# Optimization experiments

Measured on AMD Instinct MI355X. Metric: run time of the kernel, lower is better.

## Reference

```python
import jax, jax.numpy as jnp
import numpy as np

N_IMG = 8
IMG_H = IMG_W = 1024
STRIDES = (4, 8, 16, 32, 64)
FEAT = tuple(IMG_H // s for s in STRIDES)
RATIOS = (0.5, 1.0, 2.0)
A = len(RATIOS)
PRE_NMS = 1000
POST_NMS = 1000
NMS_THRESH = 0.7
SCORE_THRESH = 0.0
MIN_SIZE = 1e-3
BBOX_CLIP = float(np.log(1000.0 / 16.0))  # torchvision bbox_xform_clip
NPL = tuple(f * f * A for f in FEAT)      # anchors per level


def _make_anchors():
    levels = []
    for stride, f in zip(STRIDES, FEAT):
        size = stride * 8.0
        base = []
        for r in RATIOS:
            w = size * np.sqrt(1.0 / r)
            h = size * np.sqrt(r)
            base.append([-w / 2, -h / 2, w / 2, h / 2])
        base = np.asarray(base, np.float32)              # [A,4]
        coords = np.arange(f, dtype=np.float32) * stride
        sy, sx = np.meshgrid(coords, coords, indexing="ij")
        shifts = np.stack([sx, sy, sx, sy], -1).reshape(-1, 1, 4)  # y-major, matches [H,W,A] flatten
        levels.append((shifts + base[None]).reshape(-1, 4))
    return np.concatenate(levels, 0).astype(np.float32)


def setup_inputs() -> dict:
    key = jax.random.key(0)
    ks = jax.random.split(key, 10)
    inp = {}
    for i, f in enumerate(FEAT):
        inp[f"obj_l{i}"] = jax.random.normal(ks[i], (N_IMG, A, f, f), jnp.float32)
        inp[f"delta_l{i}"] = jax.random.normal(ks[5 + i], (N_IMG, A * 4, f, f), jnp.float32) * 0.2
    inp["anchors"] = jnp.asarray(_make_anchors())
    return inp


def _flatten_level(obj, delta):
    # permute_and_flatten: [N,A,H,W] -> [N,H*W*A] ; [N,A*4,H,W] -> [N,H*W*A,4]
    n, a, h, w = obj.shape
    o = jnp.transpose(obj, (0, 2, 3, 1)).reshape(n, -1)
    d = jnp.transpose(delta.reshape(n, a, 4, h, w), (0, 3, 4, 1, 2)).reshape(n, -1, 4)
    return o, d


def _decode(deltas, anchors):
    # BoxCoder(weights=(1,1,1,1)).decode
    w = anchors[:, 2] - anchors[:, 0]
    h = anchors[:, 3] - anchors[:, 1]
    cx = anchors[:, 0] + 0.5 * w
    cy = anchors[:, 1] + 0.5 * h
    dx, dy = deltas[..., 0], deltas[..., 1]
    dw = jnp.minimum(deltas[..., 2], BBOX_CLIP)
    dh = jnp.minimum(deltas[..., 3], BBOX_CLIP)
    pcx = dx * w + cx
    pcy = dy * h + cy
    pw = jnp.exp(dw) * w
    ph = jnp.exp(dh) * h
    return jnp.stack([pcx - 0.5 * pw, pcy - 0.5 * ph, pcx + 0.5 * pw, pcy + 0.5 * ph], -1)


def _nms_image(boxes, scores, lvl):
    # clip_boxes_to_image
    x1 = jnp.clip(boxes[:, 0], 0.0, IMG_W)
    y1 = jnp.clip(boxes[:, 1], 0.0, IMG_H)
    x2 = jnp.clip(boxes[:, 2], 0.0, IMG_W)
    y2 = jnp.clip(boxes[:, 3], 0.0, IMG_H)
    boxes = jnp.stack([x1, y1, x2, y2], -1)
    # remove_small_boxes + score_thresh, as a mask (fixed shapes)
    valid = (x2 - x1 >= MIN_SIZE) & (y2 - y1 >= MIN_SIZE) & (scores >= SCORE_THRESH)
    s = jnp.where(valid, scores, -1.0)
    order = jnp.argsort(-s)
    boxes, s, valid, lvl = boxes[order], s[order], valid[order], lvl[order]
    # batched_nms: offset boxes per level so cross-level IoU is 0
    ob = boxes + (lvl.astype(boxes.dtype) * (max(IMG_H, IMG_W) + 1.0))[:, None]
    ob = jax.lax.stop_gradient(ob)  # keep decisions are non-differentiable
    area = (ob[:, 2] - ob[:, 0]) * (ob[:, 3] - ob[:, 1])
    lt = jnp.maximum(ob[:, None, :2], ob[None, :, :2])
    rb = jnp.minimum(ob[:, None, 2:], ob[None, :, 2:])
    wh = jnp.maximum(rb - lt, 0.0)
    inter = wh[..., 0] * wh[..., 1]
    iou = inter / (area[:, None] + area[None, :] - inter + 1e-9)  # [K,K]
    k = boxes.shape[0]
    jidx = jnp.arange(k)

    def body(i, keep):
        sup = keep[i] & (iou[i] > NMS_THRESH) & (jidx > i)
        return keep & ~sup

    keep = jax.lax.fori_loop(0, k, body, valid)
    # compact kept boxes (score-sorted) into fixed [POST_NMS] output, zero-padded
    rank = jnp.cumsum(keep) - 1
    tgt = jnp.where(keep & (rank < POST_NMS), rank, POST_NMS)
    out_b = jnp.zeros((POST_NMS + 1, 4), boxes.dtype).at[tgt].set(boxes)[:POST_NMS]
    out_s = jnp.zeros((POST_NMS + 1,), s.dtype).at[tgt].set(jnp.where(keep, s, 0.0))[:POST_NMS]
    return out_b, out_s


def _forward(objs, deltas, anchors):
    flat = [_flatten_level(o, d) for o, d in zip(objs, deltas)]
    obj = jnp.concatenate([f[0] for f in flat], 1)       # [N, K_total]
    dl = jnp.concatenate([f[1] for f in flat], 1)        # [N, K_total, 4]
    proposals = _decode(dl, anchors)                     # [N, K_total, 4]
    lvl_full = jnp.concatenate([jnp.full((n,), i, jnp.int32) for i, n in enumerate(NPL)])
    # per-level top-k on objectness logits
    idxs, off = [], 0
    for n in NPL:
        kk = min(PRE_NMS, n)
        _, ti = jax.lax.top_k(obj[:, off:off + n], kk)
        idxs.append(ti + off)
        off += n
    top_idx = jnp.concatenate(idxs, 1)                   # [N, K_sel]
    scores = jax.nn.sigmoid(jnp.take_along_axis(obj, top_idx, 1))
    prop = jnp.take_along_axis(proposals, top_idx[..., None], 1)
    lvl = lvl_full[top_idx]
    boxes_out, _ = jax.lax.map(lambda t: _nms_image(*t), (prop, scores, lvl))
    return boxes_out                                     # [N, POST_NMS, 4]


def reference(obj_l0, obj_l1, obj_l2, obj_l3, obj_l4, delta_l0, delta_l1, delta_l2, delta_l3, delta_l4, anchors):
    return _forward([obj_l0, obj_l1, obj_l2, obj_l3, obj_l4],
                    [delta_l0, delta_l1, delta_l2, delta_l3, delta_l4], anchors)
```

## Files before the change

### kernel.cpp

```cpp
#include <hip/hip_runtime.h>
#include <cstdint>

#define K_SEL 4768
#define NBIN 4096
#define BUFCAP 512
#define SLICE 512
#define TPAD 9216

struct P5 { const float* p[5]; };

__device__ __forceinline__ unsigned fsortkey(float f) {
  unsigned b = __float_as_uint(f);
  return (b & 0x80000000u) ? ~b : (b | 0x80000000u);
}

__global__ __launch_bounds__(256) void k_hist(P5 obj, unsigned* phist) {
  int p = blockIdx.y; int img = p / 5, lvl = p % 5;
  int f = 256 >> lvl; int n = 3 * f * f;
  __shared__ unsigned lh[NBIN];
  for (int b = threadIdx.x; b < NBIN; b += 256) lh[b] = 0;
  __syncthreads();
  const float4* src4 = (const float4*)(obj.p[lvl] + (size_t)img * n);
  int n4 = n >> 2;
  int chunk = (n4 + gridDim.x - 1) / gridDim.x;
  int e0 = blockIdx.x * chunk, e1 = min(n4, e0 + chunk);
  for (int e = e0 + threadIdx.x; e < e1; e += 256) {
    float4 v = src4[e];
    atomicAdd(&lh[fsortkey(v.x) >> 20], 1u);
    atomicAdd(&lh[fsortkey(v.y) >> 20], 1u);
    atomicAdd(&lh[fsortkey(v.z) >> 20], 1u);
    atomicAdd(&lh[fsortkey(v.w) >> 20], 1u);
  }
  __syncthreads();
  unsigned* dst = phist + ((size_t)(p * 8 + blockIdx.x)) * NBIN;
  for (int b = threadIdx.x; b < NBIN; b += 256) dst[b] = lh[b];
}

__global__ __launch_bounds__(256) void k_thresh(const unsigned* phist, int* Bthr) {
  int p = blockIdx.x; int lvl = p % 5;
  unsigned kk = (lvl == 4) ? 768u : 1000u;
  __shared__ unsigned hsum[NBIN];
  __shared__ unsigned csum[256];
  int c = threadIdx.x;
  unsigned tot[16];
#pragma unroll
  for (int k = 0; k < 16; ++k) tot[k] = 0;
  for (int g = 0; g < 8; ++g) {
    const unsigned* hp = phist + ((size_t)(p * 8 + g)) * NBIN + c * 16;
#pragma unroll
    for (int k = 0; k < 16; ++k) tot[k] += hp[k];
  }
  unsigned s = 0;
#pragma unroll
  for (int k = 0; k < 16; ++k) { hsum[c * 16 + k] = tot[k]; s += tot[k]; }
  csum[c] = s;
  __syncthreads();
  if (c == 0) {
    unsigned acc = 0; int B = 0;
    for (int cc = 255; cc >= 0; --cc) {
      if (acc + csum[cc] >= kk) {
        for (int b = 15; b >= 0; --b) {
          acc += hsum[cc * 16 + b];
          if (acc >= kk) { B = cc * 16 + b; break; }
        }
        break;
      }
      acc += csum[cc];
    }
    Bthr[p] = B;
  }
}

__global__ __launch_bounds__(256) void k_gather(P5 obj, const int* Bthr,
                                                unsigned* cntB, unsigned long long* ck) {
  int p = blockIdx.y; int img = p / 5, lvl = p % 5;
  int f = 256 >> lvl; int hw = f * f; int n = 3 * hw;
  int B = Bthr[p];
  int tid = threadIdx.x;
  int lane = tid & 63, wv = tid >> 6;
  int shift = 2 * (8 - lvl);
  const float4* src4 = (const float4*)(obj.p[lvl] + (size_t)img * n);
  int n4 = n >> 2;
  int chunk = (n4 + 31) >> 5;
  int e0 = blockIdx.x * chunk, e1 = min(n4, e0 + chunk);
  __shared__ unsigned long long buf[4][BUFCAP];
  __shared__ unsigned wTot[4];
  unsigned wc = 0;
  for (int e = e0 + tid; e < e1; e += 256) {
    float4 v = src4[e];
    float vv[4] = {v.x, v.y, v.z, v.w};
#pragma unroll
    for (int j = 0; j < 4; ++j) {
      unsigned sv = fsortkey(vv[j]);
      bool pass = (int)(sv >> 20) >= B;
      unsigned long long m = __ballot(pass);
      if (m) {
        if (pass) {
          unsigned pos = wc + (unsigned)__popcll(m & ((1ULL << lane) - 1ULL));
          int ee = e * 4 + j;
          int a = ee >> shift;
          int r = ee & (hw - 1);
          unsigned kidx = (unsigned)(r * 3 + a);
          unsigned long long key = ((unsigned long long)sv << 32) | (0xFFFFFFFFu - kidx);
          if (pos < BUFCAP) buf[wv][pos] = key;
        }
        wc += (unsigned)__popcll(m);
      }
    }
  }
  if (lane == 0) wTot[wv] = min(wc, (unsigned)BUFCAP);
  __syncthreads();
  unsigned myOff = 0;
  for (int x = 0; x < wv; ++x) myOff += wTot[x];
  unsigned tot4 = wTot[0] + wTot[1] + wTot[2] + wTot[3];
  unsigned long long* dst = ck + ((size_t)p * 32 + blockIdx.x) * SLICE;
  for (unsigned j = lane; j < wTot[wv]; j += 64) {
    unsigned gp = myOff + j;
    if (gp < SLICE) dst[gp] = buf[wv][j];
  }
  if (tid == 0) cntB[p * 32 + blockIdx.x] = min(tot4, (unsigned)SLICE);
}

__global__ __launch_bounds__(256) void k_seldec(P5 del, const float* anchors,
                                                const unsigned* cntB,
                                                const unsigned long long* ck,
                                                float* boxP, unsigned long long* keyP) {
  int p = blockIdx.y; int img = p / 5, lvl = p % 5;
  int kk = (lvl == 4) ? 768 : 1000;
  int soff = lvl * 1000;
  int tid = threadIdx.x;
  __shared__ unsigned long long sk[4096];
  __shared__ unsigned offs[33];
  if (tid < 32) {
    unsigned v = cntB[p * 32 + tid];
#pragma unroll
    for (int d = 1; d < 32; d <<= 1) {
      unsigned o = __shfl(v, tid - d);
      if (tid >= d) v += o;
    }
    offs[tid + 1] = v;
    if (tid == 0) offs[0] = 0;
  }
  __syncthreads();
  int Cc = min((int)offs[32], 4096);
  if (blockIdx.x * 256 >= Cc) return;
  for (int x = tid; x < Cc; x += 256) {
    int lo = 0;
#pragma unroll
    for (int d = 16; d; d >>= 1)
      if (offs[lo + d] <= (unsigned)x) lo += d;
    sk[x] = ck[((size_t)p * 32 + lo) * SLICE + (x - offs[lo])];
  }
  __syncthreads();
  int c = blockIdx.x * 256 + tid;
  if (c >= Cc) return;
  unsigned long long kc = sk[c];
  unsigned k = 0xFFFFFFFFu - (unsigned)kc;
  unsigned sv = (unsigned)(kc >> 32);
  int f = 256 >> lvl, hw = f * f;
  const int aoffA[5] = {0, 196608, 245760, 258048, 261120};
  int a = (int)(k % 3u); int r = (int)(k / 3u);
  int y = r >> (8 - lvl); int x = r & (f - 1);
  const float* dp = del.p[lvl] + (size_t)(img * 12 + a * 4) * hw + (size_t)y * f + x;
  float d0 = dp[0], d1 = dp[hw], d2 = dp[2 * hw], d3 = dp[3 * hw];
  const float* ar = anchors + (size_t)(aoffA[lvl] + (int)k) * 4;
  float a0 = ar[0], a1 = ar[1], a2 = ar[2], a3 = ar[3];
  int rank = 0;
#pragma unroll 8
  for (int j = 0; j < Cc; ++j) rank += (sk[j] > kc) ? 1 : 0;
  if (rank >= kk) return;
  int i = soff + rank;
  int slot = img * K_SEL + i;
  float w = __fsub_rn(a2, a0), h = __fsub_rn(a3, a1);
  float cx = __fadd_rn(a0, __fmul_rn(0.5f, w));
  float cy = __fadd_rn(a1, __fmul_rn(0.5f, h));
  const float CLIP = 4.135166556742356f;
  float dw = fminf(d2, CLIP), dh = fminf(d3, CLIP);
  float pcx = __fadd_rn(__fmul_rn(d0, w), cx);
  float pcy = __fadd_rn(__fmul_rn(d1, h), cy);
  float pw = __fmul_rn(expf(dw), w);
  float ph = __fmul_rn(expf(dh), h);
  float x1 = __fsub_rn(pcx, __fmul_rn(0.5f, pw));
  float y1 = __fsub_rn(pcy, __fmul_rn(0.5f, ph));
  float x2 = __fadd_rn(pcx, __fmul_rn(0.5f, pw));
  float y2 = __fadd_rn(pcy, __fmul_rn(0.5f, ph));
  float x1c = fminf(fmaxf(x1, 0.0f), 1024.0f);
  float y1c = fminf(fmaxf(y1, 0.0f), 1024.0f);
  float x2c = fminf(fmaxf(x2, 0.0f), 1024.0f);
  float y2c = fminf(fmaxf(y2, 0.0f), 1024.0f);
  bool valid = (__fsub_rn(x2c, x1c) >= 1e-3f) && (__fsub_rn(y2c, y1c) >= 1e-3f);
  float* bp = boxP + (size_t)slot * 4;
  bp[0] = x1c; bp[1] = y1c; bp[2] = x2c; bp[3] = y2c;
  unsigned low = 0xFFFFFFFFu - (unsigned)i;
  keyP[slot] = valid ? (((unsigned long long)sv << 32) | low) : (unsigned long long)low;
}

__device__ __forceinline__ bool iou_gt(float rx1, float ry1, float rx2, float ry2, float rar,
                                       float cx1, float cy1, float cx2, float cy2, float car) {
  float ltx = fmaxf(rx1, cx1), lty = fmaxf(ry1, cy1);
  float rbx = fminf(rx2, cx2), rby = fminf(ry2, cy2);
  float wx = fmaxf(__fsub_rn(rbx, ltx), 0.0f);
  float wy = fmaxf(__fsub_rn(rby, lty), 0.0f);
  float inter = __fmul_rn(wx, wy);
  float denom = __fadd_rn(__fsub_rn(__fadd_rn(rar, car), inter), 1e-9f);
  return __fdiv_rn(inter, denom) > 0.7f;
}

__global__ __launch_bounds__(64) void k_lvlmask(const float* boxP, unsigned long long* T) {
  int img = blockIdx.y;
  int q = blockIdx.x;
  int lvl, q2;
  if (q < 544) { lvl = q / 136; q2 = q - lvl * 136; }
  else         { lvl = 4;       q2 = q - 544; }
  int kk = (lvl == 4) ? 768 : 1000;
  int nch = (kk + 63) >> 6;
  int rb = 0;
  while (q2 >= nch - rb) { q2 -= nch - rb; ++rb; }
  int cb = rb + q2;
  int t = threadIdx.x;
  float off = __fmul_rn((float)lvl, 1025.0f);
  const float4* b4 = (const float4*)boxP + (size_t)img * K_SEL + lvl * 1000;
  __shared__ float rx1s[64], ry1s[64], rx2s[64], ry2s[64], rars[64];
  int j = rb * 64 + t;
  if (j < kk) {
    float4 bb = b4[j];
    float ox1 = __fadd_rn(bb.x, off), oy1 = __fadd_rn(bb.y, off);
    float ox2 = __fadd_rn(bb.z, off), oy2 = __fadd_rn(bb.w, off);
    rx1s[t] = ox1; ry1s[t] = oy1; rx2s[t] = ox2; ry2s[t] = oy2;
    rars[t] = __fmul_rn(__fsub_rn(ox2, ox1), __fsub_rn(oy2, oy1));
  }
  __syncthreads();
  int i = cb * 64 + t;
  if (i >= kk) return;
  float4 bb = b4[i];
  float cx1 = __fadd_rn(bb.x, off), cy1 = __fadd_rn(bb.y, off);
  float cx2 = __fadd_rn(bb.z, off), cy2 = __fadd_rn(bb.w, off);
  float car = __fmul_rn(__fsub_rn(cx2, cx1), __fsub_rn(cy2, cy1));
  int jmaxR = min(64, kk - rb * 64);
  int jend = (rb == cb) ? min(t, jmaxR) : jmaxR;
  unsigned long long bits = 0;
  for (int jj = 0; jj < jend; ++jj) {
    if (iou_gt(rx1s[jj], ry1s[jj], rx2s[jj], ry2s[jj], rars[jj], cx1, cy1, cx2, cy2, car))
      bits |= (1ULL << jj);
  }
  const int Pt[16] = {0, 1, 4, 7, 12, 17, 24, 31, 40, 49, 60, 71, 84, 97, 112, 127};
  int sc = (cb + 1) | 1;
  T[(size_t)(img * 5 + lvl) * TPAD + 64 * Pt[cb] + t * sc + rb] = bits;
}

__global__ __launch_bounds__(256) void k_lvlnms(const unsigned long long* keyP,
                                                const unsigned long long* Tg_,
                                                unsigned long long* keepw) {
  int p = blockIdx.x; int img = p / 5, lvl = p % 5;
  int kk = (lvl == 4) ? 768 : 1000;
  int tw = (lvl == 4) ? 5376 : TPAD;
  int tid = threadIdx.x;
  __shared__ __align__(16) unsigned long long Ts[TPAD];
  const unsigned long long* Tg = Tg_ + (size_t)p * TPAD;
  const unsigned long long* kp = keyP + (size_t)img * K_SEL + lvl * 1000;
  unsigned vmask = 0;
  if (tid < 64) {
#pragma unroll
    for (int c = 0; c < 16; ++c) {
      int i = c * 64 + tid;
      bool v = (i < kk) && ((kp[min(i, kk - 1)] >> 32) != 0ULL);
      vmask |= v ? (1u << c) : 0u;
    }
  }
  {
    const ulonglong2* Tg2 = (const ulonglong2*)Tg;
    ulonglong2* Ts2 = (ulonglong2*)Ts;
    int nv = tw >> 1;
    for (int x = tid; x < nv; x += 1024) {
      int x1i = x + 256, x2i = x + 512, x3i = x + 768;
      ulonglong2 a0 = Tg2[x], a1 = {}, a2 = {}, a3 = {};
      if (x1i < nv) a1 = Tg2[x1i];
      if (x2i < nv) a2 = Tg2[x2i];
      if (x3i < nv) a3 = Tg2[x3i];
      Ts2[x] = a0;
      if (x1i < nv) Ts2[x1i] = a1;
      if (x2i < nv) Ts2[x2i] = a2;
      if (x3i < nv) Ts2[x3i] = a3;
    }
  }
  __syncthreads();
  if (tid >= 64) return;
  int t = tid;
  const int Pt[16] = {0, 1, 4, 7, 12, 17, 24, 31, 40, 49, 60, 71, 84, 97, 112, 127};
  unsigned long long kw[16];
#pragma unroll
  for (int w = 0; w < 16; ++w) kw[w] = 0ULL;
#pragma unroll
  for (int c = 0; c < 16; ++c) {
    if (c * 64 < kk) {
      int base = 64 * Pt[c] + t * ((c + 1) | 1);
      unsigned long long tv[16];
#pragma unroll
      for (int w = 0; w < 16; ++w) tv[w] = Ts[base + w];
      unsigned long long a = 0;
#pragma unroll
      for (int w = 0; w < 16; ++w) a |= tv[w] & kw[w];
      unsigned long long colT = tv[c];
      bool alive = ((vmask >> c) & 1u) && (a == 0ULL);
      unsigned long long keepm = 0ULL;
      unsigned long long actm = __ballot(alive);
      while (actm) {
        bool cank = alive && ((colT & actm) == 0ULL);
        unsigned long long newk = __ballot(cank);
        keepm |= newk;
        alive = alive && !cank && ((colT & newk) == 0ULL);
        actm = __ballot(alive);
      }
      kw[c] = keepm;
    }
  }
  if (t == 0) {
#pragma unroll
    for (int c = 0; c < 16; ++c) keepw[(size_t)p * 16 + c] = kw[c];
  }
}

__global__ __launch_bounds__(256) void k_merge(const unsigned long long* keyP, const float* boxP,
                                               const unsigned long long* keepw, float* out) {
  int p = blockIdx.x; int img = p / 5, lvl = p % 5;
  int tid = threadIdx.x;
  __shared__ unsigned long long lkey[5000];
  __shared__ int lpos[5000];
  __shared__ int wp[5][17];
  __shared__ unsigned long long kwS[80];
  for (int x = tid; x < 80; x += 256) {
    kwS[x] = keepw[(size_t)img * 80 + x];
  }
  __syncthreads();
  if (tid < 5) {
    int acc = 0;
    for (int w = 0; w < 16; ++w) { wp[tid][w] = acc; acc += (int)__popcll(kwS[tid * 16 + w]); }
    wp[tid][16] = acc;
  }
  __syncthreads();
  const unsigned long long* kp = keyP + (size_t)img * K_SEL;
  for (int i = tid; i < K_SEL; i += 256) {
    int l = (i < 4000) ? i / 1000 : 4;
    int li = i - l * 1000;
    unsigned long long wmask = kwS[l * 16 + (li >> 6)];
    if ((wmask >> (li & 63)) & 1ULL) {
      int j = wp[l][li >> 6] + (int)__popcll(wmask & ((1ULL << (li & 63)) - 1ULL));
      lkey[l * 1000 + j] = kp[i];
      lpos[l * 1000 + j] = i;
    }
  }
  __syncthreads();
  const float4* b4 = (const float4*)boxP + (size_t)img * K_SEL;
  float4* out4 = (float4*)out + (size_t)img * 1000;
  int kn = wp[lvl][16];
  for (int j = tid; j < kn; j += 256) {
    unsigned long long key = lkey[lvl * 1000 + j];
    int grank = j;
#pragma unroll
    for (int l2 = 0; l2 < 5; ++l2) {
      if (l2 == lvl) continue;
      int lo = 0, hi = wp[l2][16];
      const unsigned long long* a = &lkey[l2 * 1000];
      while (lo < hi) { int mid = (lo + hi) >> 1; if (a[mid] > key) lo = mid + 1; else hi = mid; }
      grank += lo;
    }
    if (grank < 1000) out4[grank] = b4[lpos[lvl * 1000 + j]];
  }
  if (lvl == 0) {
    int KT = wp[0][16] + wp[1][16] + wp[2][16] + wp[3][16] + wp[4][16];
    for (int s = min(KT, 1000) + tid; s < 1000; s += 256)
      out4[s] = make_float4(0.f, 0.f, 0.f, 0.f);
  }
}

extern "C" void kernel_launch(void* const* d_in, const int* in_sizes, int n_in,
                              void* d_out, int out_size, void* d_ws, size_t ws_size,
                              hipStream_t stream) {
  (void)in_sizes; (void)n_in;
  P5 obj, del;
  for (int i = 0; i < 5; ++i) {
    obj.p[i] = (const float*)d_in[2 * i];
    del.p[i] = (const float*)d_in[2 * i + 1];
  }
  const float* anchors = (const float*)d_in[10];
  float* out = (float*)d_out;
  char* ws = (char*)d_ws;

  unsigned* cntB              = (unsigned*)(ws + 0);
  int* Bthr                   = (int*)(ws + 5120);
  unsigned long long* candK   = (unsigned long long*)(ws + 8192);
  float* boxP                 = (float*)(ws + 5548544);
  unsigned long long* keyP    = (unsigned long long*)(ws + 6158848);
  unsigned long long* keepw   = (unsigned long long*)(ws + 6464000);
  unsigned long long* T       = (unsigned long long*)(ws + 6469120);
  unsigned* phist             = (unsigned*)(ws + 6469120);
  const size_t NEED = 11712000ULL;
  if (ws_size < NEED) { hipMemsetAsync(d_out, 0, (size_t)out_size * 4, stream); return; }

  k_hist    <<<dim3(8, 40), 256, 0, stream>>>(obj, phist);
  k_thresh  <<<40, 256, 0, stream>>>(phist, Bthr);
  k_gather  <<<dim3(32, 40), 256, 0, stream>>>(obj, Bthr, cntB, candK);
  k_seldec  <<<dim3(16, 40), 256, 0, stream>>>(del, anchors, cntB, candK, boxP, keyP);
  k_lvlmask <<<dim3(622, 8), 64, 0, stream>>>(boxP, T);
  k_lvlnms  <<<40, 256, 0, stream>>>(keyP, T, keepw);
  k_merge   <<<40, 256, 0, stream>>>(keyP, boxP, keepw, out);
}
```

Baseline: 203.8 us.

## Replace O(C^2) rank counting with histogram-bucketed counting sort in seldec

The selection kernel used to rank each candidate by comparing it against all other candidates, an O(C^2) scan repeated across 16 blocks per image-level. It now exports cumulative coarse-histogram counts from the threshold kernel and builds a finer sub-histogram for the boundary bin inside seldec. Candidates are scattered into buckets so each one only compares against its own bucket. The launch drops to one block per image-level with 18 candidates per thread held in registers, which lowers parallelism and raises register and LDS pressure.

```diff
diff --git a/kernel.cpp b/kernel.cpp
--- a/kernel.cpp
+++ b/kernel.cpp
@@ -5,6 +5,8 @@
 #define NBIN 4096
 #define BUFCAP 512
 #define SLICE 512
+#define CAP 4608
+#define CPT 18
 #define TPAD 9216
 
 struct P5 { const float* p[5]; };
@@ -36,11 +38,13 @@
   for (int b = threadIdx.x; b < NBIN; b += 256) dst[b] = lh[b];
 }
 
-__global__ __launch_bounds__(256) void k_thresh(const unsigned* phist, int* Bthr) {
+__global__ __launch_bounds__(256) void k_thresh(const unsigned* phist, int* Bthr,
+                                                unsigned* cumA) {
   int p = blockIdx.x; int lvl = p % 5;
   unsigned kk = (lvl == 4) ? 768u : 1000u;
   __shared__ unsigned hsum[NBIN];
   __shared__ unsigned csum[256];
+  __shared__ unsigned sAb[256];
   int c = threadIdx.x;
   unsigned tot[16];
 #pragma unroll
@@ -68,6 +72,16 @@
       acc += csum[cc];
     }
     Bthr[p] = B;
+    unsigned a2 = 0;
+    for (int cc = 255; cc >= 0; --cc) { sAb[cc] = a2; a2 += csum[cc]; }
+  }
+  __syncthreads();
+  unsigned run = sAb[c];
+  unsigned* cg = cumA + (size_t)p * NBIN;
+  for (int k = 15; k >= 0; --k) {
+    int bin = c * 16 + k;
+    cg[bin] = run;
+    run += hsum[bin];
   }
 }
 
@@ -122,15 +136,21 @@
 }
 
 __global__ __launch_bounds__(256) void k_seldec(P5 del, const float* anchors,
+                                                const int* Bthr, const unsigned* cumA,
                                                 const unsigned* cntB,
                                                 const unsigned long long* ck,
                                                 float* boxP, unsigned long long* keyP) {
-  int p = blockIdx.y; int img = p / 5, lvl = p % 5;
+  int p = blockIdx.x; int img = p / 5, lvl = p % 5;
   int kk = (lvl == 4) ? 768 : 1000;
   int soff = lvl * 1000;
   int tid = threadIdx.x;
-  __shared__ unsigned long long sk[4096];
+  __shared__ unsigned long long skS[CAP];
+  __shared__ unsigned cur1[NBIN];
+  __shared__ unsigned h2[NBIN];
+  __shared__ unsigned part[256];
   __shared__ unsigned offs[33];
+  const unsigned* cA = cumA + (size_t)p * NBIN;
+  for (int x = tid; x < NBIN; x += 256) { cur1[x] = cA[x]; h2[x] = 0u; }
   if (tid < 32) {
     unsigned v = cntB[p * 32 + tid];
 #pragma unroll
@@ -142,57 +162,121 @@
     if (tid == 0) offs[0] = 0;
   }
   __syncthreads();
-  int Cc = min((int)offs[32], 4096);
-  if (blockIdx.x * 256 >= Cc) return;
-  for (int x = tid; x < Cc; x += 256) {
-    int lo = 0;
-#pragma unroll
-    for (int d = 16; d; d >>= 1)
-      if (offs[lo + d] <= (unsigned)x) lo += d;
-    sk[x] = ck[((size_t)p * 32 + lo) * SLICE + (x - offs[lo])];
-  }
-  __syncthreads();
-  int c = blockIdx.x * 256 + tid;
-  if (c >= Cc) return;
-  unsigned long long kc = sk[c];
-  unsigned k = 0xFFFFFFFFu - (unsigned)kc;
-  unsigned sv = (unsigned)(kc >> 32);
-  int f = 256 >> lvl, hw = f * f;
-  const int aoffA[5] = {0, 196608, 245760, 258048, 261120};
-  int a = (int)(k % 3u); int r = (int)(k / 3u);
-  int y = r >> (8 - lvl); int x = r & (f - 1);
-  const float* dp = del.p[lvl] + (size_t)(img * 12 + a * 4) * hw + (size_t)y * f + x;
-  float d0 = dp[0], d1 = dp[hw], d2 = dp[2 * hw], d3 = dp[3 * hw];
-  const float* ar = anchors + (size_t)(aoffA[lvl] + (int)k) * 4;
-  float a0 = ar[0], a1 = ar[1], a2 = ar[2], a3 = ar[3];
-  int rank = 0;
-#pragma unroll 8
-  for (int j = 0; j < Cc; ++j) rank += (sk[j] > kc) ? 1 : 0;
-  if (rank >= kk) return;
-  int i = soff + rank;
-  int slot = img * K_SEL + i;
-  float w = __fsub_rn(a2, a0), h = __fsub_rn(a3, a1);
-  float cx = __fadd_rn(a0, __fmul_rn(0.5f, w));
-  float cy = __fadd_rn(a1, __fmul_rn(0.5f, h));
-  const float CLIP = 4.135166556742356f;
-  float dw = fminf(d2, CLIP), dh = fminf(d3, CLIP);
-  float pcx = __fadd_rn(__fmul_rn(d0, w), cx);
-  float pcy = __fadd_rn(__fmul_rn(d1, h), cy);
-  float pw = __fmul_rn(expf(dw), w);
-  float ph = __fmul_rn(expf(dh), h);
-  float x1 = __fsub_rn(pcx, __fmul_rn(0.5f, pw));
-  float y1 = __fsub_rn(pcy, __fmul_rn(0.5f, ph));
-  float x2 = __fadd_rn(pcx, __fmul_rn(0.5f, pw));
-  float y2 = __fadd_rn(pcy, __fmul_rn(0.5f, ph));
-  float x1c = fminf(fmaxf(x1, 0.0f), 1024.0f);
-  float y1c = fminf(fmaxf(y1, 0.0f), 1024.0f);
-  float x2c = fminf(fmaxf(x2, 0.0f), 1024.0f);
-  float y2c = fminf(fmaxf(y2, 0.0f), 1024.0f);
-  bool valid = (__fsub_rn(x2c, x1c) >= 1e-3f) && (__fsub_rn(y2c, y1c) >= 1e-3f);
-  float* bp = boxP + (size_t)slot * 4;
-  bp[0] = x1c; bp[1] = y1c; bp[2] = x2c; bp[3] = y2c;
-  unsigned low = 0xFFFFFFFFu - (unsigned)i;
-  keyP[slot] = valid ? (((unsigned long long)sv << 32) | low) : (unsigned long long)low;
+  int B = Bthr[p];
+  unsigned H = cA[B];
+  int Cc = min((int)offs[32], CAP);
+  unsigned long long key_[CPT];
+#pragma unroll
+  for (int k = 0; k < CPT; ++k) {
+    int x = tid + k * 256;
+    key_[k] = 0ULL;
+    if (x < Cc) {
+      int lo = 0;
+#pragma unroll
+      for (int d = 16; d; d >>= 1)
+        if (offs[lo + d] <= (unsigned)x) lo += d;
+      key_[k] = ck[((size_t)p * 32 + lo) * SLICE + (x - offs[lo])];
+    }
+  }
+#pragma unroll
+  for (int k = 0; k < CPT; ++k) {
+    int x = tid + k * 256;
+    if (x < Cc) {
+      unsigned sv = (unsigned)(key_[k] >> 32);
+      if ((int)(sv >> 20) == B) atomicAdd(&h2[(sv >> 8) & 0xFFFu], 1u);
+    }
+  }
+  __syncthreads();
+  {
+    unsigned s = 0;
+    for (int k2 = 0; k2 < 16; ++k2) s += h2[tid * 16 + k2];
+    part[tid] = s;
+    __syncthreads();
+    if (tid == 0) {
+      unsigned acc = 0;
+      for (int c = 255; c >= 0; --c) { unsigned t = part[c]; part[c] = acc; acc += t; }
+    }
+    __syncthreads();
+    unsigned run = part[tid];
+    for (int k2 = 15; k2 >= 0; --k2) {
+      unsigned hv = h2[tid * 16 + k2];
+      h2[tid * 16 + k2] = run;
+      run += hv;
+    }
+  }
+  __syncthreads();
+  int st_[CPT];
+#pragma unroll
+  for (int k = 0; k < CPT; ++k) {
+    int x = tid + k * 256;
+    st_[k] = 0;
+    if (x < Cc) {
+      unsigned sv = (unsigned)(key_[k] >> 32);
+      int b = (int)(sv >> 20);
+      st_[k] = (b == B) ? (int)(H + h2[(sv >> 8) & 0xFFFu]) : (int)cur1[b];
+    }
+  }
+  __syncthreads();
+  int pos_[CPT];
+#pragma unroll
+  for (int k = 0; k < CPT; ++k) {
+    int x = tid + k * 256;
+    pos_[k] = -1;
+    if (x < Cc) {
+      unsigned sv = (unsigned)(key_[k] >> 32);
+      int b = (int)(sv >> 20);
+      unsigned pos = (b == B) ? H + atomicAdd(&h2[(sv >> 8) & 0xFFFu], 1u)
+                              : atomicAdd(&cur1[b], 1u);
+      if (pos < (unsigned)CAP) { skS[pos] = key_[k]; pos_[k] = (int)pos; }
+    }
+  }
+  __syncthreads();
+#pragma unroll
+  for (int k = 0; k < CPT; ++k) {
+    if (pos_[k] < 0) continue;
+    unsigned long long kc = key_[k];
+    unsigned sv = (unsigned)(kc >> 32);
+    int b = (int)(sv >> 20);
+    int en = (b == B) ? (int)(H + h2[(sv >> 8) & 0xFFFu]) : (int)cur1[b];
+    if (en > CAP) en = CAP;
+    int st = st_[k];
+    int rank = st;
+    for (int j = st; j < en; ++j) rank += (skS[j] > kc) ? 1 : 0;
+    if (rank >= kk) continue;
+    unsigned kx = 0xFFFFFFFFu - (unsigned)kc;
+    int i = soff + rank;
+    int slot = img * K_SEL + i;
+    int f = 256 >> lvl, hw = f * f;
+    const int aoffA[5] = {0, 196608, 245760, 258048, 261120};
+    int a = (int)(kx % 3u); int r = (int)(kx / 3u);
+    int y = r >> (8 - lvl); int xi = r & (f - 1);
+    const float* dp = del.p[lvl] + (size_t)(img * 12 + a * 4) * hw + (size_t)y * f + xi;
+    float d0 = dp[0], d1 = dp[hw], d2 = dp[2 * hw], d3 = dp[3 * hw];
+    const float* ar = anchors + (size_t)(aoffA[lvl] + (int)kx) * 4;
+    float a0 = ar[0], a1 = ar[1], a2 = ar[2], a3 = ar[3];
+    float w = __fsub_rn(a2, a0), h = __fsub_rn(a3, a1);
+    float cx = __fadd_rn(a0, __fmul_rn(0.5f, w));
+    float cy = __fadd_rn(a1, __fmul_rn(0.5f, h));
+    const float CLIP = 4.135166556742356f;
+    float dw = fminf(d2, CLIP), dh = fminf(d3, CLIP);
+    float pcx = __fadd_rn(__fmul_rn(d0, w), cx);
+    float pcy = __fadd_rn(__fmul_rn(d1, h), cy);
+    float pw = __fmul_rn(expf(dw), w);
+    float ph = __fmul_rn(expf(dh), h);
+    float x1 = __fsub_rn(pcx, __fmul_rn(0.5f, pw));
+    float y1 = __fsub_rn(pcy, __fmul_rn(0.5f, ph));
+    float x2 = __fadd_rn(pcx, __fmul_rn(0.5f, pw));
+    float y2 = __fadd_rn(pcy, __fmul_rn(0.5f, ph));
+    float x1c = fminf(fmaxf(x1, 0.0f), 1024.0f);
+    float y1c = fminf(fmaxf(y1, 0.0f), 1024.0f);
+    float x2c = fminf(fmaxf(x2, 0.0f), 1024.0f);
+    float y2c = fminf(fmaxf(y2, 0.0f), 1024.0f);
+    bool valid = (__fsub_rn(x2c, x1c) >= 1e-3f) && (__fsub_rn(y2c, y1c) >= 1e-3f);
+    float* bp = boxP + (size_t)slot * 4;
+    bp[0] = x1c; bp[1] = y1c; bp[2] = x2c; bp[3] = y2c;
+    unsigned low = 0xFFFFFFFFu - (unsigned)i;
+    keyP[slot] = valid ? (((unsigned long long)sv << 32) | low) : (unsigned long long)low;
+  }
 }
 
 __device__ __forceinline__ bool iou_gt(float rx1, float ry1, float rx2, float ry2, float rar,
@@ -388,19 +472,20 @@
 
   unsigned* cntB              = (unsigned*)(ws + 0);
   int* Bthr                   = (int*)(ws + 5120);
-  unsigned long long* candK   = (unsigned long long*)(ws + 8192);
-  float* boxP                 = (float*)(ws + 5548544);
-  unsigned long long* keyP    = (unsigned long long*)(ws + 6158848);
-  unsigned long long* keepw   = (unsigned long long*)(ws + 6464000);
-  unsigned long long* T       = (unsigned long long*)(ws + 6469120);
-  unsigned* phist             = (unsigned*)(ws + 6469120);
-  const size_t NEED = 11712000ULL;
+  unsigned* cumA              = (unsigned*)(ws + 5376);
+  unsigned long long* candK   = (unsigned long long*)(ws + 663552);
+  float* boxP                 = (float*)(ws + 5906432);
+  unsigned long long* keyP    = (unsigned long long*)(ws + 6516736);
+  unsigned long long* keepw   = (unsigned long long*)(ws + 6821888);
+  unsigned long long* T       = (unsigned long long*)(ws + 6827008);
+  unsigned* phist             = (unsigned*)(ws + 6827008);
+  const size_t NEED = 12069888ULL;
   if (ws_size < NEED) { hipMemsetAsync(d_out, 0, (size_t)out_size * 4, stream); return; }
 
   k_hist    <<<dim3(8, 40), 256, 0, stream>>>(obj, phist);
-  k_thresh  <<<40, 256, 0, stream>>>(phist, Bthr);
+  k_thresh  <<<40, 256, 0, stream>>>(phist, Bthr, cumA);
   k_gather  <<<dim3(32, 40), 256, 0, stream>>>(obj, Bthr, cntB, candK);
-  k_seldec  <<<dim3(16, 40), 256, 0, stream>>>(del, anchors, cntB, candK, boxP, keyP);
+  k_seldec  <<<40, 256, 0, stream>>>(del, anchors, Bthr, cumA, cntB, candK, boxP, keyP);
   k_lvlmask <<<dim3(622, 8), 64, 0, stream>>>(boxP, T);
   k_lvlnms  <<<40, 256, 0, stream>>>(keyP, T, keepw);
   k_merge   <<<40, 256, 0, stream>>>(keyP, boxP, keepw, out);
```

Result: slower. 273.5 us (+34.2%).

## Add second-level radix histogram to shrink candidate set before rank selection

Applied to the files above, without the earlier changes.

Adds a k_thresh2 kernel that builds a finer 12-bit histogram over candidates falling in the boundary coarse bin, which gives a tighter threshold. k_seldec then compacts only the surviving candidates into shared memory before running the O(C^2) rank loop, and launches half as many blocks. The goal is to cut the quadratic rank-counting work and shared-memory footprint. The cost is an extra kernel launch and an extra pass reading the candidate keys.

```diff
diff --git a/kernel.cpp b/kernel.cpp
--- a/kernel.cpp
+++ b/kernel.cpp
@@ -5,6 +5,9 @@
 #define NBIN 4096
 #define BUFCAP 512
 #define SLICE 512
+#define CAPR 4608
+#define CPT 18
+#define CAP2 2048
 #define TPAD 9216
 
 struct P5 { const float* p[5]; };
@@ -36,7 +39,8 @@
   for (int b = threadIdx.x; b < NBIN; b += 256) dst[b] = lh[b];
 }
 
-__global__ __launch_bounds__(256) void k_thresh(const unsigned* phist, int* Bthr) {
+__global__ __launch_bounds__(256) void k_thresh(const unsigned* phist, int* Bthr,
+                                                unsigned* Hthr) {
   int p = blockIdx.x; int lvl = p % 5;
   unsigned kk = (lvl == 4) ? 768u : 1000u;
   __shared__ unsigned hsum[NBIN];
@@ -56,10 +60,11 @@
   csum[c] = s;
   __syncthreads();
   if (c == 0) {
-    unsigned acc = 0; int B = 0;
+    unsigned acc = 0, H = 0; int B = 0;
     for (int cc = 255; cc >= 0; --cc) {
       if (acc + csum[cc] >= kk) {
         for (int b = 15; b >= 0; --b) {
+          H = acc;
           acc += hsum[cc * 16 + b];
           if (acc >= kk) { B = cc * 16 + b; break; }
         }
@@ -68,6 +73,7 @@
       acc += csum[cc];
     }
     Bthr[p] = B;
+    Hthr[p] = H;
   }
 }
 
@@ -121,7 +127,66 @@
   if (tid == 0) cntB[p * 32 + blockIdx.x] = min(tot4, (unsigned)SLICE);
 }
 
+__global__ __launch_bounds__(256) void k_thresh2(const int* Bthr, const unsigned* Hthr,
+                                                 const unsigned* cntB,
+                                                 const unsigned long long* ck,
+                                                 int* B2thr, unsigned* Cc2g) {
+  int p = blockIdx.x; int lvl = p % 5;
+  unsigned kk = (lvl == 4) ? 768u : 1000u;
+  int B1 = Bthr[p];
+  unsigned H = Hthr[p];
+  unsigned kk2 = kk - H;
+  int tid = threadIdx.x;
+  __shared__ unsigned h2[NBIN];
+  __shared__ unsigned csum[256];
+  __shared__ unsigned offs[33];
+  for (int x = tid; x < NBIN; x += 256) h2[x] = 0;
+  if (tid < 32) {
+    unsigned v = cntB[p * 32 + tid];
+#pragma unroll
+    for (int d = 1; d < 32; d <<= 1) {
+      unsigned o = __shfl(v, tid - d);
+      if (tid >= d) v += o;
+    }
+    offs[tid + 1] = v;
+    if (tid == 0) offs[0] = 0;
+  }
+  __syncthreads();
+  int Cc = min((int)offs[32], CAPR);
+  for (int x = tid; x < Cc; x += 256) {
+    int lo = 0;
+#pragma unroll
+    for (int d = 16; d; d >>= 1)
+      if (offs[lo + d] <= (unsigned)x) lo += d;
+    unsigned long long key = ck[((size_t)p * 32 + lo) * SLICE + (x - offs[lo])];
+    unsigned sv = (unsigned)(key >> 32);
+    if ((int)(sv >> 20) == B1) atomicAdd(&h2[(sv >> 8) & 0xFFFu], 1u);
+  }
+  __syncthreads();
+  unsigned s = 0;
+  for (int k = 0; k < 16; ++k) s += h2[tid * 16 + k];
+  csum[tid] = s;
+  __syncthreads();
+  if (tid == 0) {
+    unsigned acc = 0; int B2 = 0;
+    for (int cc = 255; cc >= 0; --cc) {
+      if (acc + csum[cc] >= kk2) {
+        for (int b = 15; b >= 0; --b) {
+          acc += h2[cc * 16 + b];
+          if (acc >= kk2) { B2 = cc * 16 + b; break; }
+        }
+        break;
+      }
+      acc += csum[cc];
+    }
+    B2thr[p] = B2;
+    Cc2g[p] = H + acc;
+  }
+}
+
 __global__ __launch_bounds__(256) void k_seldec(P5 del, const float* anchors,
+                                                const int* Bthr, const int* B2thr,
+                                                const unsigned* Cc2g,
                                                 const unsigned* cntB,
                                                 const unsigned long long* ck,
                                                 float* boxP, unsigned long long* keyP) {
@@ -129,8 +194,12 @@
   int kk = (lvl == 4) ? 768 : 1000;
   int soff = lvl * 1000;
   int tid = threadIdx.x;
-  __shared__ unsigned long long sk[4096];
+  int lane = tid & 63, wv = tid >> 6;
+  unsigned Cc2 = min(Cc2g[p], (unsigned)CAP2);
+  if ((unsigned)(blockIdx.x * 256) >= Cc2) return;
+  __shared__ unsigned long long skc[CAP2];
   __shared__ unsigned offs[33];
+  __shared__ unsigned wsum[4];
   if (tid < 32) {
     unsigned v = cntB[p * 32 + tid];
 #pragma unroll
@@ -142,32 +211,61 @@
     if (tid == 0) offs[0] = 0;
   }
   __syncthreads();
-  int Cc = min((int)offs[32], 4096);
-  if (blockIdx.x * 256 >= Cc) return;
-  for (int x = tid; x < Cc; x += 256) {
-    int lo = 0;
-#pragma unroll
-    for (int d = 16; d; d >>= 1)
-      if (offs[lo + d] <= (unsigned)x) lo += d;
-    sk[x] = ck[((size_t)p * 32 + lo) * SLICE + (x - offs[lo])];
-  }
-  __syncthreads();
+  int B1 = Bthr[p], B2 = B2thr[p];
+  int Cc = min((int)offs[32], CAPR);
+  unsigned long long key_[CPT];
+  bool sur_[CPT];
+  unsigned myc = 0;
+#pragma unroll
+  for (int k = 0; k < CPT; ++k) {
+    int x = tid + k * 256;
+    key_[k] = 0ULL; sur_[k] = false;
+    if (x < Cc) {
+      int lo = 0;
+#pragma unroll
+      for (int d = 16; d; d >>= 1)
+        if (offs[lo + d] <= (unsigned)x) lo += d;
+      key_[k] = ck[((size_t)p * 32 + lo) * SLICE + (x - offs[lo])];
+      unsigned sv = (unsigned)(key_[k] >> 32);
+      int b = (int)(sv >> 20);
+      sur_[k] = (b > B1) || (b == B1 && (int)((sv >> 8) & 0xFFFu) >= B2);
+      myc += sur_[k] ? 1u : 0u;
+    }
+  }
+  unsigned v = myc;
+#pragma unroll
+  for (int d = 1; d < 64; d <<= 1) {
+    unsigned o = __shfl(v, lane - d);
+    if (lane >= d) v += o;
+  }
+  if (lane == 63) wsum[wv] = v;
+  __syncthreads();
+  unsigned base = 0;
+  for (int x = 0; x < wv; ++x) base += wsum[x];
+  unsigned pos = base + v - myc;
+  unsigned Ccc = wsum[0] + wsum[1] + wsum[2] + wsum[3];
+#pragma unroll
+  for (int k = 0; k < CPT; ++k) {
+    if (sur_[k]) { if (pos < (unsigned)CAP2) skc[pos] = key_[k]; ++pos; }
+  }
+  __syncthreads();
+  int Cs = min((int)Ccc, CAP2);
   int c = blockIdx.x * 256 + tid;
-  if (c >= Cc) return;
-  unsigned long long kc = sk[c];
-  unsigned k = 0xFFFFFFFFu - (unsigned)kc;
+  if (c >= Cs) return;
+  unsigned long long kc = skc[c];
+  unsigned kx = 0xFFFFFFFFu - (unsigned)kc;
   unsigned sv = (unsigned)(kc >> 32);
   int f = 256 >> lvl, hw = f * f;
   const int aoffA[5] = {0, 196608, 245760, 258048, 261120};
-  int a = (int)(k % 3u); int r = (int)(k / 3u);
-  int y = r >> (8 - lvl); int x = r & (f - 1);
-  const float* dp = del.p[lvl] + (size_t)(img * 12 + a * 4) * hw + (size_t)y * f + x;
+  int a = (int)(kx % 3u); int r = (int)(kx / 3u);
+  int y = r >> (8 - lvl); int xi = r & (f - 1);
+  const float* dp = del.p[lvl] + (size_t)(img * 12 + a * 4) * hw + (size_t)y * f + xi;
   float d0 = dp[0], d1 = dp[hw], d2 = dp[2 * hw], d3 = dp[3 * hw];
-  const float* ar = anchors + (size_t)(aoffA[lvl] + (int)k) * 4;
+  const float* ar = anchors + (size_t)(aoffA[lvl] + (int)kx) * 4;
   float a0 = ar[0], a1 = ar[1], a2 = ar[2], a3 = ar[3];
   int rank = 0;
 #pragma unroll 8
-  for (int j = 0; j < Cc; ++j) rank += (sk[j] > kc) ? 1 : 0;
+  for (int j = 0; j < Cs; ++j) rank += (skc[j] > kc) ? 1 : 0;
   if (rank >= kk) return;
   int i = soff + rank;
   int slot = img * K_SEL + i;
@@ -388,6 +486,9 @@
 
   unsigned* cntB              = (unsigned*)(ws + 0);
   int* Bthr                   = (int*)(ws + 5120);
+  unsigned* Hthr              = (unsigned*)(ws + 5280);
+  int* B2thr                  = (int*)(ws + 5440);
+  unsigned* Cc2g              = (unsigned*)(ws + 5600);
   unsigned long long* candK   = (unsigned long long*)(ws + 8192);
   float* boxP                 = (float*)(ws + 5548544);
   unsigned long long* keyP    = (unsigned long long*)(ws + 6158848);
@@ -398,9 +499,11 @@
   if (ws_size < NEED) { hipMemsetAsync(d_out, 0, (size_t)out_size * 4, stream); return; }
 
   k_hist    <<<dim3(8, 40), 256, 0, stream>>>(obj, phist);
-  k_thresh  <<<40, 256, 0, stream>>>(phist, Bthr);
+  k_thresh  <<<40, 256, 0, stream>>>(phist, Bthr, Hthr);
   k_gather  <<<dim3(32, 40), 256, 0, stream>>>(obj, Bthr, cntB, candK);
-  k_seldec  <<<dim3(16, 40), 256, 0, stream>>>(del, anchors, cntB, candK, boxP, keyP);
+  k_thresh2 <<<40, 256, 0, stream>>>(Bthr, Hthr, cntB, candK, B2thr, Cc2g);
+  k_seldec  <<<dim3(8, 40), 256, 0, stream>>>(del, anchors, Bthr, B2thr, Cc2g, cntB,
+                                              candK, boxP, keyP);
   k_lvlmask <<<dim3(622, 8), 64, 0, stream>>>(boxP, T);
   k_lvlnms  <<<40, 256, 0, stream>>>(keyP, T, keepw);
   k_merge   <<<40, 256, 0, stream>>>(keyP, boxP, keepw, out);
```

Result: slower. 218.1 us (+7.0%).
